# Optimization experiments

Measured on AMD Instinct MI355X. Metric: run time of the kernel, lower is better.

## Reference

```python
import jax, jax.numpy as jnp
import numpy as np

N_EMBD = 64
HEAD_SIZE = 64
BLOCK_SIZE = 256


def setup_inputs() -> dict:
    key = jax.random.key(0)
    ks = jax.random.split(key, 7)
    B, T = 1024, 256
    inputs = jax.random.normal(ks[0], (B, T, N_EMBD), dtype=jnp.float32)
    s = 1.0 / np.sqrt(N_EMBD)
    Wq = jax.random.uniform(ks[1], (HEAD_SIZE, N_EMBD), jnp.float32, -s, s)
    Wk = jax.random.uniform(ks[2], (HEAD_SIZE, N_EMBD), jnp.float32, -s, s)
    Wv = jax.random.uniform(ks[3], (HEAD_SIZE, N_EMBD), jnp.float32, -s, s)
    bq = jax.random.uniform(ks[4], (HEAD_SIZE,), jnp.float32, -s, s)
    bk = jax.random.uniform(ks[5], (HEAD_SIZE,), jnp.float32, -s, s)
    bv = jax.random.uniform(ks[6], (HEAD_SIZE,), jnp.float32, -s, s)
    return {"inputs": inputs, "Wq": Wq, "bq": bq, "Wk": Wk, "bk": bk, "Wv": Wv, "bv": bv}


def reference(inputs, Wq, bq, Wk, bk, Wv, bv):
    # inputs: [B, T, C]; Linear weights stored torch-style [out, in]
    T = inputs.shape[1]
    Q = jnp.einsum('btc,hc->bth', inputs, Wq) + bq  # [B,T,H]
    K = jnp.einsum('btc,hc->bth', inputs, Wk) + bk
    V = jnp.einsum('btc,hc->bth', inputs, Wv) + bv
    scale = 1.0 / jnp.sqrt(jnp.float32(K.shape[-1]))
    scores = jnp.einsum('bth,bsh->bts', Q, K) * scale  # [B,T,T]
    causal = jnp.triu(jnp.ones((T, T), dtype=bool), k=1)
    scores = jnp.where(causal, jnp.float32(-1e9), scores)
    attn = jax.nn.softmax(scores, axis=-1)
    return jnp.einsum('bts,bsh->bth', attn, V)
```

## Files before the change

kernel.cpp:

```cpp
#include <hip/hip_runtime.h>

typedef __attribute__((ext_vector_type(8))) __bf16 bf16x8;
typedef __attribute__((ext_vector_type(4))) float f32x4;
typedef __attribute__((ext_vector_type(4))) unsigned int u32x4;
typedef __attribute__((ext_vector_type(2))) unsigned int u32x2;

#define LDS_SCR 0
#define LDS_K   10240
#define LDS_VT  43008
#define LDS_TOT 75776
#define W_Q (LDS_VT)
#define W_K (LDS_VT + 8192)
#define W_V (LDS_VT + 16384)

#define QSCALE 0.180336880f

static __device__ __forceinline__ float exp2g(float x) {
#if __has_builtin(__builtin_amdgcn_exp2f)
  return __builtin_amdgcn_exp2f(x);
#else
  return exp2f(x);
#endif
}
static __device__ __forceinline__ unsigned int cvt_pk_bf16(float a, float b) {
  unsigned int r;
  asm("v_cvt_pk_bf16_f32 %0, %1, %2" : "=v"(r) : "v"(a), "v"(b));
  return r;
}
static __device__ __forceinline__ int swz128(int row, int colbyte) {
  return row * 128 + (colbyte ^ ((row & 7) << 4));
}
static __device__ __forceinline__ int swz512(int row, int colbyte) {
  return row * 512 + (colbyte ^ ((row & 7) << 4));
}
static __device__ __forceinline__ bf16x8 ldx(const float* p) {
  const float4* p4 = (const float4*)p;
  float4 lo = p4[0], hi = p4[1];
  u32x4 u;
  u.x = cvt_pk_bf16(lo.x, lo.y); u.y = cvt_pk_bf16(lo.z, lo.w);
  u.z = cvt_pk_bf16(hi.x, hi.y); u.w = cvt_pk_bf16(hi.z, hi.w);
  return __builtin_bit_cast(bf16x8, u);
}

static __device__ __forceinline__ void qk_unit(const char* smemK, int ln, int g,
    bf16x8 q0, bf16x8 q1, int jt, f32x4 (&s)[4])
{
#pragma unroll
  for (int nk = 0; nk < 4; ++nk) s[nk] = (f32x4){0.f, 0.f, 0.f, 0.f};
  __builtin_amdgcn_s_setprio(1);
#pragma unroll
  for (int ks = 0; ks < 2; ++ks) {
    bf16x8 qk = ks ? q1 : q0;
    bf16x8 kb[4];
#pragma unroll
    for (int nk = 0; nk < 4; ++nk) {
      u32x4 u = *(const u32x4*)(smemK + swz128(jt * 64 + nk * 16 + ln, (ks * 32 + g * 8) * 2));
      kb[nk] = __builtin_bit_cast(bf16x8, u);
    }
#pragma unroll
    for (int nk = 0; nk < 4; ++nk)
      s[nk] = __builtin_amdgcn_mfma_f32_16x16x32_bf16(kb[nk], qk, s[nk], 0, 0, 0);
  }
  __builtin_amdgcn_s_setprio(0);
}
static __device__ __forceinline__ void mask_unit(f32x4 (&s)[4], int jt, int q_abs, int g)
{
#pragma unroll
  for (int nk = 0; nk < 4; ++nk) {
    int keybase = jt * 64 + nk * 16 + g * 4;
#pragma unroll
    for (int d = 0; d < 4; ++d)
      s[nk][d] = (keybase + d > q_abs) ? -1e30f : s[nk][d];
  }
}
static __device__ __forceinline__ void exp_unit(f32x4 (&s)[4], float& lpart)
{
  float sum = 0.f;
#pragma unroll
  for (int nk = 0; nk < 4; ++nk)
#pragma unroll
    for (int d = 0; d < 4; ++d) {
      float p = exp2g(s[nk][d]);
      s[nk][d] = p;
      sum += p;
    }
  lpart += sum;
}
static __device__ __forceinline__ void pv_unit(char* scr, const char* smemVT, int ln, int g,
                                               int jt, f32x4 (&s)[4], f32x4 (&oacc)[4])
{
#pragma unroll
  for (int h2 = 0; h2 < 2; ++h2) {
#pragma unroll
    for (int n2 = 0; n2 < 2; ++n2) {
      f32x4 sv = s[h2 * 2 + n2];
      u32x2 p;
      p.x = cvt_pk_bf16(sv[0], sv[1]);
      p.y = cvt_pk_bf16(sv[2], sv[3]);
      *(u32x2*)(scr + ln * 80 + n2 * 32 + g * 8) = p;
    }
    bf16x8 pa;
    {
      u32x4 u = *(const u32x4*)(scr + ln * 80 + g * 16);
      pa = __builtin_bit_cast(bf16x8, u);
    }
    bf16x8 vb[4];
#pragma unroll
    for (int nf = 0; nf < 4; ++nf) {
      int key0 = jt * 64 + h2 * 32 + g * 8;
      u32x4 u = *(const u32x4*)(smemVT + swz512(nf * 16 + ln, key0 * 2));
      vb[nf] = __builtin_bit_cast(bf16x8, u);
    }
    __builtin_amdgcn_s_setprio(1);
#pragma unroll
    for (int nf = 0; nf < 4; ++nf)
      oacc[nf] = __builtin_amdgcn_mfma_f32_16x16x32_bf16(pa, vb[nf], oacc[nf], 0, 0, 0);
    __builtin_amdgcn_s_setprio(0);
  }
}
static __device__ __forceinline__ void epi_unit(float* og, f32x4 (&oacc)[4], float lpart,
                                                int qbase, int ln, int g)
{
  float lsum = lpart;
  lsum += __shfl_xor(lsum, 16);
  lsum += __shfl_xor(lsum, 32);
  float linv = 1.0f / lsum;
  float inv[4];
#pragma unroll
  for (int d = 0; d < 4; ++d) inv[d] = __shfl(linv, g * 4 + d);
#pragma unroll
  for (int nf = 0; nf < 4; ++nf)
#pragma unroll
    for (int d = 0; d < 4; ++d) {
      int t = qbase + g * 4 + d;
      og[t * 64 + nf * 16 + ln] = oacc[nf][d] * inv[d];
    }
}

__global__ __launch_bounds__(512, 4)
void head_fused(const float* __restrict__ x,
                const float* __restrict__ Wq, const float* __restrict__ bq,
                const float* __restrict__ Wk, const float* __restrict__ bk,
                const float* __restrict__ Wv, const float* __restrict__ bv,
                float* __restrict__ out)
{
  __shared__ __align__(16) char smem[LDS_TOT];
  const int b    = blockIdx.x;
  const int tid  = threadIdx.x;
  const int lane = tid & 63;
  const int wid  = tid >> 6;
  const int g    = lane >> 4;
  const int ln   = lane & 15;
  const int tA   = wid;
  const int tB   = 15 - wid;

  const float* xb = x + (size_t)b * (256 * 64);
  char* scr = smem + LDS_SCR + wid * 1280;

  bf16x8 xfA[2], xfB[2];
#pragma unroll
  for (int ks = 0; ks < 2; ++ks) {
    xfA[ks] = ldx(xb + (tA * 16 + ln) * 64 + ks * 32 + g * 8);
    xfB[ks] = ldx(xb + (tB * 16 + ln) * 64 + ks * 32 + g * 8);
  }

#pragma unroll
  for (int i = 0; i < 6; ++i) {
    int idx = tid + i * 512;
    int mat = idx >> 10;
    int rem = idx & 1023;
    const float4* wg = (const float4*)(mat == 0 ? Wq : (mat == 1 ? Wk : Wv));
    float4 v = wg[rem];
    int e = rem * 4;
    int h = e >> 6, c = e & 63;
    u32x2 p;
    p.x = cvt_pk_bf16(v.x, v.y);
    p.y = cvt_pk_bf16(v.z, v.w);
    *(u32x2*)(smem + W_Q + mat * 8192 + swz128(h, c * 2)) = p;
  }
  __syncthreads();

  bf16x8 qaA[2], qaB[2];
#pragma unroll
  for (int ti = 0; ti < 2; ++ti) {
    bf16x8 xf0 = ti ? xfB[0] : xfA[0];
    bf16x8 xf1 = ti ? xfB[1] : xfA[1];
#pragma unroll
    for (int hk = 0; hk < 2; ++hk) {
#pragma unroll
      for (int mt2 = 0; mt2 < 2; ++mt2) {
        int mt = hk * 2 + mt2;
        float4 bb = *(const float4*)(bq + mt * 16 + g * 4);
        f32x4 acc = {0.f, 0.f, 0.f, 0.f};
        {
          u32x4 u = *(const u32x4*)(smem + W_Q + swz128(mt * 16 + ln, (0 * 32 + g * 8) * 2));
          acc = __builtin_amdgcn_mfma_f32_16x16x32_bf16(__builtin_bit_cast(bf16x8, u), xf0, acc, 0, 0, 0);
        }
        {
          u32x4 u = *(const u32x4*)(smem + W_Q + swz128(mt * 16 + ln, (1 * 32 + g * 8) * 2));
          acc = __builtin_amdgcn_mfma_f32_16x16x32_bf16(__builtin_bit_cast(bf16x8, u), xf1, acc, 0, 0, 0);
        }
        u32x2 p;
        p.x = cvt_pk_bf16((acc[0] + bb.x) * QSCALE, (acc[1] + bb.y) * QSCALE);
        p.y = cvt_pk_bf16((acc[2] + bb.z) * QSCALE, (acc[3] + bb.w) * QSCALE);
        *(u32x2*)(scr + ln * 80 + mt2 * 32 + g * 8) = p;
      }
      u32x4 u = *(const u32x4*)(scr + ln * 80 + g * 16);
      if (ti) qaB[hk] = __builtin_bit_cast(bf16x8, u);
      else    qaA[hk] = __builtin_bit_cast(bf16x8, u);
    }
  }

#pragma unroll
  for (int ti = 0; ti < 2; ++ti) {
    int tile = ti ? tB : tA;
    bf16x8 xf0 = ti ? xfB[0] : xfA[0];
    bf16x8 xf1 = ti ? xfB[1] : xfA[1];
#pragma unroll
    for (int mt = 0; mt < 4; ++mt) {
      float4 bb = *(const float4*)(bk + mt * 16 + g * 4);
      f32x4 acc = {0.f, 0.f, 0.f, 0.f};
      {
        u32x4 u = *(const u32x4*)(smem + W_K + swz128(mt * 16 + ln, (0 * 32 + g * 8) * 2));
        acc = __builtin_amdgcn_mfma_f32_16x16x32_bf16(__builtin_bit_cast(bf16x8, u), xf0, acc, 0, 0, 0);
      }
      {
        u32x4 u = *(const u32x4*)(smem + W_K + swz128(mt * 16 + ln, (1 * 32 + g * 8) * 2));
        acc = __builtin_amdgcn_mfma_f32_16x16x32_bf16(__builtin_bit_cast(bf16x8, u), xf1, acc, 0, 0, 0);
      }
      u32x2 p;
      p.x = cvt_pk_bf16(acc[0] + bb.x, acc[1] + bb.y);
      p.y = cvt_pk_bf16(acc[2] + bb.z, acc[3] + bb.w);
      *(u32x2*)(smem + LDS_K + swz128(tile * 16 + ln, (mt * 16 + g * 4) * 2)) = p;
    }
  }

  bf16x8 wv[4][2];
  float bvv[4];
#pragma unroll
  for (int nf = 0; nf < 4; ++nf) {
    bvv[nf] = bv[nf * 16 + ln];
#pragma unroll
    for (int ks = 0; ks < 2; ++ks) {
      u32x4 u = *(const u32x4*)(smem + W_V + swz128(nf * 16 + ln, (ks * 32 + g * 8) * 2));
      wv[nf][ks] = __builtin_bit_cast(bf16x8, u);
    }
  }
  __syncthreads();

#pragma unroll
  for (int ti = 0; ti < 2; ++ti) {
    int tile = ti ? tB : tA;
    bf16x8 xf0 = ti ? xfB[0] : xfA[0];
    bf16x8 xf1 = ti ? xfB[1] : xfA[1];
#pragma unroll
    for (int nf = 0; nf < 4; ++nf) {
      f32x4 acc = {0.f, 0.f, 0.f, 0.f};
      acc = __builtin_amdgcn_mfma_f32_16x16x32_bf16(xf0, wv[nf][0], acc, 0, 0, 0);
      acc = __builtin_amdgcn_mfma_f32_16x16x32_bf16(xf1, wv[nf][1], acc, 0, 0, 0);
      int t0 = tile * 16 + g * 4;
      u32x2 p;
      p.x = cvt_pk_bf16(acc[0] + bvv[nf], acc[1] + bvv[nf]);
      p.y = cvt_pk_bf16(acc[2] + bvv[nf], acc[3] + bvv[nf]);
      *(u32x2*)(smem + LDS_VT + swz512(nf * 16 + ln, t0 * 2)) = p;
    }
  }
  __syncthreads();

  float* og = out + (size_t)b * (256 * 64);
  const char* smemK  = smem + LDS_K;
  const char* smemVT = smem + LDS_VT;

#pragma unroll
  for (int ti = 0; ti < 2; ++ti) {
    const int tile = ti ? tB : tA;
    bf16x8 qa0 = ti ? qaB[0] : qaA[0];
    bf16x8 qa1 = ti ? qaB[1] : qaA[1];
    const int qbase = tile * 16;
    const int jmaxT = qbase >> 6;

    float lpart = 0.f;
    f32x4 oacc[4];
#pragma unroll
    for (int nf = 0; nf < 4; ++nf)
      oacc[nf] = (f32x4){0.f, 0.f, 0.f, 0.f};
    f32x4 s[4];

    for (int jt = 0; jt <= jmaxT; ++jt) {
      qk_unit(smemK, ln, g, qa0, qa1, jt, s);
      if (jt == jmaxT) mask_unit(s, jt, qbase + ln, g);
      exp_unit(s, lpart);
      pv_unit(scr, smemVT, ln, g, jt, s, oacc);
    }
    epi_unit(og, oacc, lpart, qbase, ln, g);
  }
}

extern "C" void kernel_launch(void* const* d_in, const int* in_sizes, int n_in,
                              void* d_out, int out_size, void* d_ws, size_t ws_size,
                              hipStream_t stream) {
  (void)in_sizes; (void)n_in; (void)d_ws; (void)ws_size; (void)out_size;
  const float* x  = (const float*)d_in[0];
  const float* Wq = (const float*)d_in[1];
  const float* bq = (const float*)d_in[2];
  const float* Wk = (const float*)d_in[3];
  const float* bk = (const float*)d_in[4];
  const float* Wv = (const float*)d_in[5];
  const float* bv = (const float*)d_in[6];
  float* out = (float*)d_out;
  hipLaunchKernelGGL(head_fused, dim3(1024), dim3(512), 0, stream,
                     x, Wq, bq, Wk, bk, Wv, bv, out);
}
```

Baseline: 39.75 us.

## Make kernel persistent over four batches, keeping bf16 weights resident in LDS

Launches 256 blocks instead of 1024, and each block loops over four batch elements (b, b+256, ...). The bf16-converted Q/K/V weights move to their own LDS region so they are converted once per block rather than once per batch. This cuts redundant weight loading and conversion. The cost is more LDS per block (100 KB versus 76 KB), which lowers occupancy. With 256 blocks on the GPU's 256 CUs, each CU runs one block serially, so there may be less latency hiding and less overlap.

Result: slower. 44.46 us (+11.8%).

```diff
diff --git a/kernel.cpp b/kernel.cpp
--- a/kernel.cpp
+++ b/kernel.cpp
@@ -8,10 +8,10 @@
 #define LDS_SCR 0
 #define LDS_K   10240
 #define LDS_VT  43008
-#define LDS_TOT 75776
-#define W_Q (LDS_VT)
-#define W_K (LDS_VT + 8192)
-#define W_V (LDS_VT + 16384)
+#define W_Q     75776
+#define W_K     83968
+#define W_V     92160
+#define LDS_TOT 100352
 
 #define QSCALE 0.180336880f
 
@@ -145,7 +145,6 @@
                 float* __restrict__ out)
 {
   __shared__ __align__(16) char smem[LDS_TOT];
-  const int b    = blockIdx.x;
   const int tid  = threadIdx.x;
   const int lane = tid & 63;
   const int wid  = tid >> 6;
@@ -154,15 +153,9 @@
   const int tA   = wid;
   const int tB   = 15 - wid;
 
-  const float* xb = x + (size_t)b * (256 * 64);
   char* scr = smem + LDS_SCR + wid * 1280;
-
-  bf16x8 xfA[2], xfB[2];
-#pragma unroll
-  for (int ks = 0; ks < 2; ++ks) {
-    xfA[ks] = ldx(xb + (tA * 16 + ln) * 64 + ks * 32 + g * 8);
-    xfB[ks] = ldx(xb + (tB * 16 + ln) * 64 + ks * 32 + g * 8);
-  }
+  const char* smemK  = smem + LDS_K;
+  const char* smemVT = smem + LDS_VT;
 
 #pragma unroll
   for (int i = 0; i < 6; ++i) {
@@ -178,121 +171,135 @@
     p.y = cvt_pk_bf16(v.z, v.w);
     *(u32x2*)(smem + W_Q + mat * 8192 + swz128(h, c * 2)) = p;
   }
+
+  float bvv[4];
+#pragma unroll
+  for (int nf = 0; nf < 4; ++nf) bvv[nf] = bv[nf * 16 + ln];
+
+  int b = blockIdx.x;
+  bf16x8 xfA[2], xfB[2];
+#pragma unroll
+  for (int ks = 0; ks < 2; ++ks) {
+    xfA[ks] = ldx(x + (size_t)b * 16384 + (tA * 16 + ln) * 64 + ks * 32 + g * 8);
+    xfB[ks] = ldx(x + (size_t)b * 16384 + (tB * 16 + ln) * 64 + ks * 32 + g * 8);
+  }
   __syncthreads();
 
-  bf16x8 qaA[2], qaB[2];
-#pragma unroll
-  for (int ti = 0; ti < 2; ++ti) {
-    bf16x8 xf0 = ti ? xfB[0] : xfA[0];
-    bf16x8 xf1 = ti ? xfB[1] : xfA[1];
-#pragma unroll
-    for (int hk = 0; hk < 2; ++hk) {
-#pragma unroll
-      for (int mt2 = 0; mt2 < 2; ++mt2) {
-        int mt = hk * 2 + mt2;
-        float4 bb = *(const float4*)(bq + mt * 16 + g * 4);
+  for (int bi = 0; bi < 4; ++bi) {
+    bf16x8 qaA[2], qaB[2];
+#pragma unroll
+    for (int ti = 0; ti < 2; ++ti) {
+      bf16x8 xf0 = ti ? xfB[0] : xfA[0];
+      bf16x8 xf1 = ti ? xfB[1] : xfA[1];
+#pragma unroll
+      for (int hk = 0; hk < 2; ++hk) {
+#pragma unroll
+        for (int mt2 = 0; mt2 < 2; ++mt2) {
+          int mt = hk * 2 + mt2;
+          float4 bb = *(const float4*)(bq + mt * 16 + g * 4);
+          f32x4 acc = {0.f, 0.f, 0.f, 0.f};
+          {
+            u32x4 u = *(const u32x4*)(smem + W_Q + swz128(mt * 16 + ln, (0 * 32 + g * 8) * 2));
+            acc = __builtin_amdgcn_mfma_f32_16x16x32_bf16(__builtin_bit_cast(bf16x8, u), xf0, acc, 0, 0, 0);
+          }
+          {
+            u32x4 u = *(const u32x4*)(smem + W_Q + swz128(mt * 16 + ln, (1 * 32 + g * 8) * 2));
+            acc = __builtin_amdgcn_mfma_f32_16x16x32_bf16(__builtin_bit_cast(bf16x8, u), xf1, acc, 0, 0, 0);
+          }
+          u32x2 p;
+          p.x = cvt_pk_bf16((acc[0] + bb.x) * QSCALE, (acc[1] + bb.y) * QSCALE);
+          p.y = cvt_pk_bf16((acc[2] + bb.z) * QSCALE, (acc[3] + bb.w) * QSCALE);
+          *(u32x2*)(scr + ln * 80 + mt2 * 32 + g * 8) = p;
+        }
+        u32x4 u = *(const u32x4*)(scr + ln * 80 + g * 16);
+        if (ti) qaB[hk] = __builtin_bit_cast(bf16x8, u);
+        else    qaA[hk] = __builtin_bit_cast(bf16x8, u);
+      }
+    }
+
+#pragma unroll
+    for (int ti = 0; ti < 2; ++ti) {
+      int tile = ti ? tB : tA;
+      bf16x8 xf0 = ti ? xfB[0] : xfA[0];
+      bf16x8 xf1 = ti ? xfB[1] : xfA[1];
+#pragma unroll
+      for (int mt = 0; mt < 4; ++mt) {
+        float4 bb = *(const float4*)(bk + mt * 16 + g * 4);
         f32x4 acc = {0.f, 0.f, 0.f, 0.f};
         {
-          u32x4 u = *(const u32x4*)(smem + W_Q + swz128(mt * 16 + ln, (0 * 32 + g * 8) * 2));
+          u32x4 u = *(const u32x4*)(smem + W_K + swz128(mt * 16 + ln, (0 * 32 + g * 8) * 2));
           acc = __builtin_amdgcn_mfma_f32_16x16x32_bf16(__builtin_bit_cast(bf16x8, u), xf0, acc, 0, 0, 0);
         }
         {
-          u32x4 u = *(const u32x4*)(smem + W_Q + swz128(mt * 16 + ln, (1 * 32 + g * 8) * 2));
+          u32x4 u = *(const u32x4*)(smem + W_K + swz128(mt * 16 + ln, (1 * 32 + g * 8) * 2));
           acc = __builtin_amdgcn_mfma_f32_16x16x32_bf16(__builtin_bit_cast(bf16x8, u), xf1, acc, 0, 0, 0);
         }
         u32x2 p;
-        p.x = cvt_pk_bf16((acc[0] + bb.x) * QSCALE, (acc[1] + bb.y) * QSCALE);
-        p.y = cvt_pk_bf16((acc[2] + bb.z) * QSCALE, (acc[3] + bb.w) * QSCALE);
-        *(u32x2*)(scr + ln * 80 + mt2 * 32 + g * 8) = p;
-      }
-      u32x4 u = *(const u32x4*)(scr + ln * 80 + g * 16);
-      if (ti) qaB[hk] = __builtin_bit_cast(bf16x8, u);
-      else    qaA[hk] = __builtin_bit_cast(bf16x8, u);
-    }
-  }
-
-#pragma unroll
-  for (int ti = 0; ti < 2; ++ti) {
-    int tile = ti ? tB : tA;
-    bf16x8 xf0 = ti ? xfB[0] : xfA[0];
-    bf16x8 xf1 = ti ? xfB[1] : xfA[1];
-#pragma unroll
-    for (int mt = 0; mt < 4; ++mt) {
-      float4 bb = *(const float4*)(bk + mt * 16 + g * 4);
-      f32x4 acc = {0.f, 0.f, 0.f, 0.f};
-      {
-        u32x4 u = *(const u32x4*)(smem + W_K + swz128(mt * 16 + ln, (0 * 32 + g * 8) * 2));
-        acc = __builtin_amdgcn_mfma_f32_16x16x32_bf16(__builtin_bit_cast(bf16x8, u), xf0, acc, 0, 0, 0);
-      }
-      {
-        u32x4 u = *(const u32x4*)(smem + W_K + swz128(mt * 16 + ln, (1 * 32 + g * 8) * 2));
-        acc = __builtin_amdgcn_mfma_f32_16x16x32_bf16(__builtin_bit_cast(bf16x8, u), xf1, acc, 0, 0, 0);
-      }
-      u32x2 p;
-      p.x = cvt_pk_bf16(acc[0] + bb.x, acc[1] + bb.y);
-      p.y = cvt_pk_bf16(acc[2] + bb.z, acc[3] + bb.w);
-      *(u32x2*)(smem + LDS_K + swz128(tile * 16 + ln, (mt * 16 + g * 4) * 2)) = p;
-    }
-  }
-
-  bf16x8 wv[4][2];
-  float bvv[4];
-#pragma unroll
-  for (int nf = 0; nf < 4; ++nf) {
-    bvv[nf] = bv[nf * 16 + ln];
-#pragma unroll
-    for (int ks = 0; ks < 2; ++ks) {
-      u32x4 u = *(const u32x4*)(smem + W_V + swz128(nf * 16 + ln, (ks * 32 + g * 8) * 2));
-      wv[nf][ks] = __builtin_bit_cast(bf16x8, u);
-    }
-  }
-  __syncthreads();
-
-#pragma unroll
-  for (int ti = 0; ti < 2; ++ti) {
-    int tile = ti ? tB : tA;
-    bf16x8 xf0 = ti ? xfB[0] : xfA[0];
-    bf16x8 xf1 = ti ? xfB[1] : xfA[1];
-#pragma unroll
-    for (int nf = 0; nf < 4; ++nf) {
-      f32x4 acc = {0.f, 0.f, 0.f, 0.f};
-      acc = __builtin_amdgcn_mfma_f32_16x16x32_bf16(xf0, wv[nf][0], acc, 0, 0, 0);
-      acc = __builtin_amdgcn_mfma_f32_16x16x32_bf16(xf1, wv[nf][1], acc, 0, 0, 0);
-      int t0 = tile * 16 + g * 4;
-      u32x2 p;
-      p.x = cvt_pk_bf16(acc[0] + bvv[nf], acc[1] + bvv[nf]);
-      p.y = cvt_pk_bf16(acc[2] + bvv[nf], acc[3] + bvv[nf]);
-      *(u32x2*)(smem + LDS_VT + swz512(nf * 16 + ln, t0 * 2)) = p;
-    }
-  }
-  __syncthreads();
-
-  float* og = out + (size_t)b * (256 * 64);
-  const char* smemK  = smem + LDS_K;
-  const char* smemVT = smem + LDS_VT;
-
-#pragma unroll
-  for (int ti = 0; ti < 2; ++ti) {
-    const int tile = ti ? tB : tA;
-    bf16x8 qa0 = ti ? qaB[0] : qaA[0];
-    bf16x8 qa1 = ti ? qaB[1] : qaA[1];
-    const int qbase = tile * 16;
-    const int jmaxT = qbase >> 6;
-
-    float lpart = 0.f;
-    f32x4 oacc[4];
-#pragma unroll
-    for (int nf = 0; nf < 4; ++nf)
-      oacc[nf] = (f32x4){0.f, 0.f, 0.f, 0.f};
-    f32x4 s[4];
-
-    for (int jt = 0; jt <= jmaxT; ++jt) {
-      qk_unit(smemK, ln, g, qa0, qa1, jt, s);
-      if (jt == jmaxT) mask_unit(s, jt, qbase + ln, g);
-      exp_unit(s, lpart);
-      pv_unit(scr, smemVT, ln, g, jt, s, oacc);
-    }
-    epi_unit(og, oacc, lpart, qbase, ln, g);
+        p.x = cvt_pk_bf16(acc[0] + bb.x, acc[1] + bb.y);
+        p.y = cvt_pk_bf16(acc[2] + bb.z, acc[3] + bb.w);
+        *(u32x2*)(smem + LDS_K + swz128(tile * 16 + ln, (mt * 16 + g * 4) * 2)) = p;
+      }
+    }
+
+#pragma unroll
+    for (int ti = 0; ti < 2; ++ti) {
+      int tile = ti ? tB : tA;
+      bf16x8 xf0 = ti ? xfB[0] : xfA[0];
+      bf16x8 xf1 = ti ? xfB[1] : xfA[1];
+#pragma unroll
+      for (int nf = 0; nf < 4; ++nf) {
+        f32x4 acc = {0.f, 0.f, 0.f, 0.f};
+        {
+          u32x4 u = *(const u32x4*)(smem + W_V + swz128(nf * 16 + ln, (0 * 32 + g * 8) * 2));
+          acc = __builtin_amdgcn_mfma_f32_16x16x32_bf16(xf0, __builtin_bit_cast(bf16x8, u), acc, 0, 0, 0);
+        }
+        {
+          u32x4 u = *(const u32x4*)(smem + W_V + swz128(nf * 16 + ln, (1 * 32 + g * 8) * 2));
+          acc = __builtin_amdgcn_mfma_f32_16x16x32_bf16(xf1, __builtin_bit_cast(bf16x8, u), acc, 0, 0, 0);
+        }
+        int t0 = tile * 16 + g * 4;
+        u32x2 p;
+        p.x = cvt_pk_bf16(acc[0] + bvv[nf], acc[1] + bvv[nf]);
+        p.y = cvt_pk_bf16(acc[2] + bvv[nf], acc[3] + bvv[nf]);
+        *(u32x2*)(smem + LDS_VT + swz512(nf * 16 + ln, t0 * 2)) = p;
+      }
+    }
+    __syncthreads();
+
+    float* og = out + (size_t)b * 16384;
+#pragma unroll
+    for (int ti = 0; ti < 2; ++ti) {
+      const int tile = ti ? tB : tA;
+      bf16x8 qa0 = ti ? qaB[0] : qaA[0];
+      bf16x8 qa1 = ti ? qaB[1] : qaA[1];
+      const int qbase = tile * 16;
+      const int jmaxT = qbase >> 6;
+
+      float lpart = 0.f;
+      f32x4 oacc[4];
+#pragma unroll
+      for (int nf = 0; nf < 4; ++nf)
+        oacc[nf] = (f32x4){0.f, 0.f, 0.f, 0.f};
+      f32x4 s[4];
+
+      for (int jt = 0; jt <= jmaxT; ++jt) {
+        qk_unit(smemK, ln, g, qa0, qa1, jt, s);
+        if (jt == jmaxT) mask_unit(s, jt, qbase + ln, g);
+        exp_unit(s, lpart);
+        pv_unit(scr, smemVT, ln, g, jt, s, oacc);
+      }
+      epi_unit(og, oacc, lpart, qbase, ln, g);
+    }
+
+    if (bi < 3) {
+      b += 256;
+#pragma unroll
+      for (int ks = 0; ks < 2; ++ks) {
+        xfA[ks] = ldx(x + (size_t)b * 16384 + (tA * 16 + ln) * 64 + ks * 32 + g * 8);
+        xfB[ks] = ldx(x + (size_t)b * 16384 + (tB * 16 + ln) * 64 + ks * 32 + g * 8);
+      }
+      __syncthreads();
+    }
   }
 }
 
@@ -308,6 +315,6 @@
   const float* Wv = (const float*)d_in[5];
   const float* bv = (const float*)d_in[6];
   float* out = (float*)d_out;
-  hipLaunchKernelGGL(head_fused, dim3(1024), dim3(512), 0, stream,
+  hipLaunchKernelGGL(head_fused, dim3(256), dim3(512), 0, stream,
                      x, Wq, bq, Wk, bk, Wv, bv, out);
 }
```
